# Kernel optimization log

Measured on AMD Instinct MI355X. Metric: run time of the kernel, lower is better.

The kernel has to match this reference:

```python
import jax, jax.numpy as jnp
import numpy as np

B, C_IN, V, C_OUT, K = 4, 64, 50000, 128, 7


def setup_inputs() -> dict:
    key = jax.random.key(0)
    k1, k2, k3, k4 = jax.random.split(key, 4)
    x = jax.random.normal(k1, (B, C_IN, V, 1), dtype=jnp.float32)
    # Gi: per-vertex [self, n1, n2, n3] indices (random neighbors, in-range)
    Gi = jax.random.randint(k2, (B, V, 4), 0, V, dtype=jnp.int64)
    # Conv2d(in, out, kernel=(1,7)) weight collapsed to [out, in, 7]
    W = jax.random.normal(k3, (C_OUT, C_IN, K), dtype=jnp.float32) * 0.05
    b = jax.random.normal(k4, (C_OUT,), dtype=jnp.float32) * 0.05
    return {"x": x, "Gi": Gi, "W": W, "b": b}


def reference(x, Gi, W, b):
    xs = x[..., 0]  # [B, C, V]  (squeeze(-1))
    Bx, C, Vx = xs.shape
    # prepend zero-padding column (index 0 after Gi+1 maps padded -1 entries)
    xp = jnp.concatenate([jnp.zeros((Bx, C, 1), xs.dtype), xs], axis=2)  # [B,C,V+1]
    gi = Gi + 1
    # gather per batch: f[b,c,v,j] = xp[b,c,gi[b,v,j]]
    f = jax.vmap(lambda xb, gb: xb[:, gb])(xp, gi)  # [B, C, V, 4]
    f0, f1, f2, f3 = f[..., 0], f[..., 1], f[..., 2], f[..., 3]
    G = jnp.stack([
        f0,
        f1 + f2 + f3,                                        # symm_oper 1
        f1 * f2 * f3,                                        # symm_oper 2
        f1 * f2 + f1 * f3 + f2 * f3,                         # symm_oper 3
        f1 * f1 + f2 * f2 + f3 * f3,                         # symm_oper 4
        jnp.abs(f1 - f2) + jnp.abs(f1 - f3) + jnp.abs(f2 - f3),  # symm_oper 5
        f1 * f1 * f1 + f2 * f2 * f2 + f3 * f3 * f3,          # symm_oper 6
    ], axis=3)  # [B, C, V, 7]
    # conv2d with kernel (1,7), no padding -> width collapses to 1
    out = jnp.einsum('bcvk,ock->bov', G, W) + b[None, :, None]
    return out[..., None]  # [B, C_out, V, 1]
```

## Files before the change

### kernel.cpp

```cpp
#include <hip/hip_runtime.h>
#include <cstdint>
#include <cstddef>

#define BB   4
#define CIN  64
#define VV   50000
#define COUT 128
#define NV   32
#define NTILES 1563
#define KTOT 448
#define KT   14
#define PITCH 456

typedef __attribute__((ext_vector_type(8))) short     short8;
typedef __attribute__((ext_vector_type(8))) _Float16  half8;
typedef __attribute__((ext_vector_type(4))) float     f32x4;

__device__ _Float16       g_xt[(size_t)BB * VV * CIN];
__device__ unsigned short g_wb[KT * 8 * 64 * 8];

__device__ inline unsigned short f2h(float f) {
    union { _Float16 h; unsigned short u; } cv;
    cv.h = (_Float16)f;
    return cv.u;
}

__global__ __launch_bounds__(256) void transpose_k(const float* __restrict__ x,
                                                   const float* __restrict__ W) {
    if (blockIdx.y == 0 && blockIdx.x < (KT * 8 * 64 + 255) / 256) {
        int idx = blockIdx.x * 256 + threadIdx.x;
        if (idx < KT * 8 * 64) {
            int lane = idx & 63;
            int mt   = (idx >> 6) & 7;
            int kt   = idx >> 9;
            int m    = mt * 16 + (lane & 15);
            int kb   = kt * 32 + (lane >> 4) * 8;
            union { unsigned short s[8]; short8 v; } u;
#pragma unroll
            for (int j = 0; j < 8; j++) {
                int kk = kb + j;
                int c  = kk & 63;
                int k  = kk >> 6;
                u.s[j] = f2h(W[((size_t)m * CIN + c) * 7 + k]);
            }
            *(short8*)&g_wb[(size_t)idx * 8] = u.v;
        }
    }

    __shared__ float tile[64][65];
    int b  = blockIdx.y;
    int v0 = blockIdx.x * 64;
    int t  = threadIdx.x;
    int tv = t & 15;
    int tc = t >> 4;
#pragma unroll
    for (int i = 0; i < 4; i++) {
        int c = tc + 16 * i;
        int v = v0 + tv * 4;
        const float* src = x + ((size_t)b * CIN + c) * VV + v;
        f32x4 f;
        if (v + 3 < VV) {
            f = __builtin_nontemporal_load((const f32x4*)src);
        } else {
            f[0] = v + 0 < VV ? src[0] : 0.f;
            f[1] = v + 1 < VV ? src[1] : 0.f;
            f[2] = v + 2 < VV ? src[2] : 0.f;
            f[3] = v + 3 < VV ? src[3] : 0.f;
        }
        tile[c][tv * 4 + 0] = f[0];
        tile[c][tv * 4 + 1] = f[1];
        tile[c][tv * 4 + 2] = f[2];
        tile[c][tv * 4 + 3] = f[3];
    }
    __syncthreads();
    int c8  = t & 7;
    int tvv = t >> 3;
#pragma unroll
    for (int i = 0; i < 2; i++) {
        int v = v0 + tvv + 32 * i;
        if (v < VV) {
            union { _Float16 h[8]; short8 s; } u;
#pragma unroll
            for (int j = 0; j < 8; j++)
                u.h[j] = (_Float16)tile[c8 * 8 + j][tvv + 32 * i];
            *(short8*)(g_xt + ((size_t)b * VV + v) * CIN + c8 * 8) = u.s;
        }
    }
}

__device__ inline void feats(float f0, float f1, float f2, float f3, float* g) {
    g[0] = f0;
    g[1] = f1 + f2 + f3;
    float p12 = f1 * f2, p13 = f1 * f3, p23 = f2 * f3;
    g[2] = p12 * f3;
    g[3] = p12 + p13 + p23;
    g[4] = f1 * f1 + f2 * f2 + f3 * f3;
    g[5] = fabsf(f1 - f2) + fabsf(f1 - f3) + fabsf(f2 - f3);
    g[6] = f1 * f1 * f1 + f2 * f2 * f2 + f3 * f3 * f3;
}

__global__ __launch_bounds__(256) void mesh_k(
        const void* __restrict__ Gi, const float* __restrict__ bias,
        float* __restrict__ out) {
    __shared__ _Float16 Gl[NV * PITCH];
    __shared__ int Sidx[NV][4];

    int bid  = blockIdx.x;
    int b    = (bid & 7) >> 1;
    int tile = ((bid >> 3) << 1) + (bid & 1);
    if (tile >= NTILES) return;
    int v0 = tile * NV;
    int t  = threadIdx.x;

    const unsigned* gu = (const unsigned*)Gi;
    bool is64 = ((gu[1] | gu[3] | gu[5] | gu[7]) == 0u);

    if (t < NV * 4) {
        int vv = t >> 2, j = t & 3;
        int v  = v0 + vv;
        long long val = 0;
        if (v < VV) {
            size_t gb = ((size_t)b * VV + v) * 4 + j;
            val = is64 ? __builtin_nontemporal_load((const long long*)Gi + gb)
                       : (long long)__builtin_nontemporal_load((const int*)Gi + gb);
        }
        Sidx[vv][j] = (int)(val < 0 ? 0 : (val >= VV ? VV - 1 : val));
    }
    __syncthreads();

    int c8   = t & 7;
    int slot = t >> 3;
    int J[4];
#pragma unroll
    for (int j = 0; j < 4; ++j) J[j] = Sidx[slot][j];

    const _Float16* base = g_xt + (size_t)b * VV * CIN + c8 * 8;
    half8 F[4];
#pragma unroll
    for (int j = 0; j < 4; ++j)
        F[j] = *(const half8*)(base + (size_t)J[j] * CIN);

    union { _Float16 h[8]; short8 s; } u[7];
#pragma unroll
    for (int i = 0; i < 8; ++i) {
        float g7[7];
        feats((float)F[0][i], (float)F[1][i], (float)F[2][i], (float)F[3][i], g7);
#pragma unroll
        for (int k = 0; k < 7; ++k) u[k].h[i] = (_Float16)g7[k];
    }
    _Float16* grow = &Gl[slot * PITCH + c8 * 8];
#pragma unroll
    for (int k = 0; k < 7; ++k)
        *(short8*)(grow + k * 64) = u[k].s;
    __syncthreads();

    int w    = t >> 6;
    int lane = t & 63;
    int l15  = lane & 15;
    int q    = lane >> 4;

    f32x4 acc[2][2] = {};

    const half8* wb = (const half8*)g_wb;
#pragma unroll 2
    for (int kt = 0; kt < KT; ++kt) {
        half8 a0 = wb[(kt * 8 + 2 * w    ) * 64 + lane];
        half8 a1 = wb[(kt * 8 + 2 * w + 1) * 64 + lane];
        half8 b0 = *(const half8*)&Gl[(l15     ) * PITCH + kt * 32 + q * 8];
        half8 b1 = *(const half8*)&Gl[(l15 + 16) * PITCH + kt * 32 + q * 8];
        acc[0][0] = __builtin_amdgcn_mfma_f32_16x16x32_f16(a0, b0, acc[0][0], 0, 0, 0);
        acc[0][1] = __builtin_amdgcn_mfma_f32_16x16x32_f16(a0, b1, acc[0][1], 0, 0, 0);
        acc[1][0] = __builtin_amdgcn_mfma_f32_16x16x32_f16(a1, b0, acc[1][0], 0, 0, 0);
        acc[1][1] = __builtin_amdgcn_mfma_f32_16x16x32_f16(a1, b1, acc[1][1], 0, 0, 0);
    }

#pragma unroll
    for (int mt = 0; mt < 2; ++mt) {
        int o = 32 * w + mt * 16 + q * 4;
        float bs[4];
#pragma unroll
        for (int r = 0; r < 4; ++r) bs[r] = bias[o + r];
#pragma unroll
        for (int n = 0; n < 2; ++n) {
            int vv = v0 + n * 16 + l15;
            if (vv < VV) {
                float* po = out + ((size_t)b * COUT + o) * VV + vv;
#pragma unroll
                for (int r = 0; r < 4; ++r)
                    __builtin_nontemporal_store(acc[mt][n][r] + bs[r], po + (size_t)r * VV);
            }
        }
    }
}

extern "C" void kernel_launch(void* const* d_in, const int* in_sizes, int n_in,
                              void* d_out, int out_size, void* d_ws, size_t ws_size,
                              hipStream_t stream) {
    const float* x    = (const float*)d_in[0];
    const void*  Gi   = d_in[1];
    const float* W    = (const float*)d_in[2];
    const float* bias = (const float*)d_in[3];
    float* out        = (float*)d_out;

    dim3 gt((VV + 63) / 64, BB);
    transpose_k<<<gt, 256, 0, stream>>>(x, W);
    mesh_k<<<dim3(8 * ((NTILES + 1) / 2)), 256, 0, stream>>>(Gi, bias, out);
}
```

Baseline: 197.6 us.

## Shuffle gather indices, prefetch weight fragments, and set occupancy hint in mesh kernel

Each wave now loads its own neighbor indices and spreads them with wave shuffles, which removes the shared-memory index table and one block barrier. The first weight fragments are loaded before the gather, and the MFMA loop is fully unrolled with next-iteration weight prefetch in registers. The mesh kernel gets a min-blocks-per-CU launch bound of 4, and the transpose kernel's x load switches from nontemporal to a normal load. These changes aim to hide global weight-load latency and cut synchronization, at the cost of more register pressure, which the occupancy hint may force into spills.

New measurement: 202.4 us. +2.4%, slower.

```diff
diff --git a/kernel.cpp b/kernel.cpp
--- a/kernel.cpp
+++ b/kernel.cpp
@@ -60,7 +60,7 @@
         const float* src = x + ((size_t)b * CIN + c) * VV + v;
         f32x4 f;
         if (v + 3 < VV) {
-            f = __builtin_nontemporal_load((const f32x4*)src);
+            f = *(const f32x4*)src;
         } else {
             f[0] = v + 0 < VV ? src[0] : 0.f;
             f[1] = v + 1 < VV ? src[1] : 0.f;
@@ -99,11 +99,10 @@
     g[6] = f1 * f1 * f1 + f2 * f2 * f2 + f3 * f3 * f3;
 }
 
-__global__ __launch_bounds__(256) void mesh_k(
+__global__ __launch_bounds__(256, 4) void mesh_k(
         const void* __restrict__ Gi, const float* __restrict__ bias,
         float* __restrict__ out) {
     __shared__ _Float16 Gl[NV * PITCH];
-    __shared__ int Sidx[NV][4];
 
     int bid  = blockIdx.x;
     int b    = (bid & 7) >> 1;
@@ -111,28 +110,36 @@
     if (tile >= NTILES) return;
     int v0 = tile * NV;
     int t  = threadIdx.x;
+    int w    = t >> 6;
+    int lane = t & 63;
 
     const unsigned* gu = (const unsigned*)Gi;
     bool is64 = ((gu[1] | gu[3] | gu[5] | gu[7]) == 0u);
 
-    if (t < NV * 4) {
-        int vv = t >> 2, j = t & 3;
+    int val = 0;
+    {
+        int vv = 8 * w + (lane >> 2);
+        int j  = lane & 3;
         int v  = v0 + vv;
-        long long val = 0;
-        if (v < VV) {
+        if (lane < 32 && v < VV) {
             size_t gb = ((size_t)b * VV + v) * 4 + j;
-            val = is64 ? __builtin_nontemporal_load((const long long*)Gi + gb)
-                       : (long long)__builtin_nontemporal_load((const int*)Gi + gb);
-        }
-        Sidx[vv][j] = (int)(val < 0 ? 0 : (val >= VV ? VV - 1 : val));
-    }
-    __syncthreads();
+            long long xv = is64 ? ((const long long*)Gi)[gb]
+                                : (long long)((const int*)Gi)[gb];
+            val = (int)(xv < 0 ? 0 : (xv >= VV ? VV - 1 : xv));
+        }
+    }
+
+    const half8* wbp = (const half8*)g_wb;
+    half8 a0c = wbp[(2 * w    ) * 64 + lane];
+    half8 a1c = wbp[(2 * w + 1) * 64 + lane];
+
+    int J[4];
+    int srcl = (lane >> 3) << 2;
+#pragma unroll
+    for (int j = 0; j < 4; ++j) J[j] = __shfl(val, srcl + j, 64);
 
     int c8   = t & 7;
     int slot = t >> 3;
-    int J[4];
-#pragma unroll
-    for (int j = 0; j < 4; ++j) J[j] = Sidx[slot][j];
 
     const _Float16* base = g_xt + (size_t)b * VV * CIN + c8 * 8;
     half8 F[4];
@@ -154,24 +161,24 @@
         *(short8*)(grow + k * 64) = u[k].s;
     __syncthreads();
 
-    int w    = t >> 6;
-    int lane = t & 63;
     int l15  = lane & 15;
     int q    = lane >> 4;
 
     f32x4 acc[2][2] = {};
-
-    const half8* wb = (const half8*)g_wb;
-#pragma unroll 2
+    half8 a0n, a1n;
+#pragma unroll
     for (int kt = 0; kt < KT; ++kt) {
-        half8 a0 = wb[(kt * 8 + 2 * w    ) * 64 + lane];
-        half8 a1 = wb[(kt * 8 + 2 * w + 1) * 64 + lane];
+        if (kt + 1 < KT) {
+            a0n = wbp[((kt + 1) * 8 + 2 * w    ) * 64 + lane];
+            a1n = wbp[((kt + 1) * 8 + 2 * w + 1) * 64 + lane];
+        }
         half8 b0 = *(const half8*)&Gl[(l15     ) * PITCH + kt * 32 + q * 8];
         half8 b1 = *(const half8*)&Gl[(l15 + 16) * PITCH + kt * 32 + q * 8];
-        acc[0][0] = __builtin_amdgcn_mfma_f32_16x16x32_f16(a0, b0, acc[0][0], 0, 0, 0);
-        acc[0][1] = __builtin_amdgcn_mfma_f32_16x16x32_f16(a0, b1, acc[0][1], 0, 0, 0);
-        acc[1][0] = __builtin_amdgcn_mfma_f32_16x16x32_f16(a1, b0, acc[1][0], 0, 0, 0);
-        acc[1][1] = __builtin_amdgcn_mfma_f32_16x16x32_f16(a1, b1, acc[1][1], 0, 0, 0);
+        acc[0][0] = __builtin_amdgcn_mfma_f32_16x16x32_f16(a0c, b0, acc[0][0], 0, 0, 0);
+        acc[0][1] = __builtin_amdgcn_mfma_f32_16x16x32_f16(a0c, b1, acc[0][1], 0, 0, 0);
+        acc[1][0] = __builtin_amdgcn_mfma_f32_16x16x32_f16(a1c, b0, acc[1][0], 0, 0, 0);
+        acc[1][1] = __builtin_amdgcn_mfma_f32_16x16x32_f16(a1c, b1, acc[1][1], 0, 0, 0);
+        a0c = a0n; a1c = a1n;
     }
 
 #pragma unroll
```
